# Kernel tuning notes

Measured on AMD Instinct MI355X. Metric: run time of the kernel, lower is better.

Reference implementation:

```python
import jax, jax.numpy as jnp
import numpy as np
from jax import lax

B, N, D, L, EDGE_H, NGNN = 8, 128, 256, 64, 64, 3


def setup_inputs() -> dict:
    key = jax.random.key(0)
    ks = iter(jax.random.split(key, 64))
    def nrm(shape, s=0.02):
        return jax.random.normal(next(ks), shape, jnp.float32) * s
    inp = {}
    inp["node_feats"] = jax.random.uniform(next(ks), (B, N, 11), jnp.float32)
    inp["edge_feats"] = jax.random.normal(next(ks), (B, N, N, 3), jnp.float32)
    inp["adj_mask"] = jax.random.randint(next(ks), (B, N, N), 0, 2).astype(bool)
    inp["layer_costs"] = jax.random.uniform(next(ks), (B, L), jnp.float32)
    inp["global_dynamic"] = jax.random.uniform(next(ks), (B, 2), jnp.float32)
    inp["p_node_w"] = nrm((11, D)); inp["p_node_b"] = jnp.zeros((D,), jnp.float32)
    inp["g_w1"] = nrm((NGNN, D + 3, EDGE_H)); inp["g_b1"] = jnp.zeros((NGNN, EDGE_H), jnp.float32)
    inp["g_w2"] = nrm((NGNN, EDGE_H, D)); inp["g_b2"] = jnp.zeros((NGNN, D), jnp.float32)
    inp["u_w1"] = nrm((NGNN, 3 * D, D)); inp["u_b1"] = jnp.zeros((NGNN, D), jnp.float32)
    inp["u_w2"] = nrm((NGNN, D, D)); inp["u_b2"] = jnp.zeros((NGNN, D), jnp.float32)
    inp["ln_g"] = jnp.ones((NGNN, D), jnp.float32); inp["ln_b"] = jnp.zeros((NGNN, D), jnp.float32)
    inp["conv_w"] = nrm((32, 1, 4)); inp["conv_b"] = jnp.zeros((32,), jnp.float32)
    inp["lp_w"] = nrm((32 * 31, D)); inp["lp_b"] = jnp.zeros((D,), jnp.float32)
    inp["q_w"] = nrm((2 * D + 2, D)); inp["q_b"] = jnp.zeros((D,), jnp.float32)
    inp["k_w"] = nrm((D, D)); inp["k_b"] = jnp.zeros((D,), jnp.float32)
    inp["s_w1"] = nrm((D + 2, D)); inp["s_b1"] = jnp.zeros((D,), jnp.float32)
    inp["s_w2"] = nrm((D, 1)); inp["s_b2"] = jnp.zeros((1,), jnp.float32)
    inp["v_w1"] = nrm((2 * D + 2, D)); inp["v_b1"] = jnp.zeros((D,), jnp.float32)
    inp["v_w2"] = nrm((D, 1)); inp["v_b2"] = jnp.zeros((1,), jnp.float32)
    return inp


def _ecgc(h, edge_feats, adj_bool, gw1, gb1, gw2, gb2, uw1, ub1, uw2, ub2, lng, lnb):
    Bh, Nn, Dd = h.shape
    # h_j: features of sender node j broadcast over receiver axis -> (B, N, N, D)
    h_j = jnp.broadcast_to(h[:, None, :, :], (Bh, Nn, Nn, Dd))
    gate_in = jnp.concatenate([h_j, edge_feats], axis=-1)            # (B,N,N,D+3)
    gates = jax.nn.sigmoid(jax.nn.relu(gate_in @ gw1 + gb1) @ gw2 + gb2)
    msg = gates * h_j                                                # (B,N,N,D)
    m = adj_bool.astype(h.dtype)[..., None]
    cnt = jnp.maximum(m.sum(axis=2), 1.0)                            # (B,N,1)
    agg_mean = (msg * m).sum(axis=2) / cnt                           # (B,N,D)
    agg_max = jnp.where(adj_bool[..., None], msg, -jnp.inf).max(axis=2)
    agg_max = jnp.where(jnp.isinf(agg_max), 0.0, agg_max)
    ui = jnp.concatenate([h, agg_mean, agg_max], axis=-1)            # (B,N,3D)
    x = h + (jax.nn.relu(ui @ uw1 + ub1) @ uw2 + ub2)
    mu = x.mean(-1, keepdims=True)
    var = ((x - mu) ** 2).mean(-1, keepdims=True)
    return (x - mu) * lax.rsqrt(var + 1e-5) * lng + lnb


def reference(node_feats, edge_feats, adj_mask, layer_costs, global_dynamic,
              p_node_w, p_node_b, g_w1, g_b1, g_w2, g_b2, u_w1, u_b1, u_w2, u_b2,
              ln_g, ln_b, conv_w, conv_b, lp_w, lp_b, q_w, q_b, k_w, k_b,
              s_w1, s_b1, s_w2, s_b2, v_w1, v_b1, v_w2, v_b2):
    # layer cost encoder: Conv1d(1,32,k=4,s=2) + ReLU, flatten, Linear
    le = lax.conv_general_dilated(layer_costs[:, None, :], conv_w, (2,), 'VALID',
                                  dimension_numbers=('NCH', 'OIH', 'NCH'))
    le = jax.nn.relu(le + conv_b[None, :, None])                     # (B,32,31)
    layer_embed = le.reshape(le.shape[0], -1) @ lp_w + lp_b          # (B,D)
    h = node_feats @ p_node_w + p_node_b                             # (B,N,D)
    for i in range(g_w1.shape[0]):
        h = _ecgc(h, edge_feats, adj_mask, g_w1[i], g_b1[i], g_w2[i], g_b2[i],
                  u_w1[i], u_b1[i], u_w2[i], u_b2[i], ln_g[i], ln_b[i])
    w = (node_feats[:, :, 0] * node_feats[:, :, 7])[..., None]       # (B,N,1)
    graph_embed = (w * h).sum(axis=1) / jnp.maximum(w.sum(axis=1), 1e-8)
    qi = jnp.concatenate([graph_embed, layer_embed, global_dynamic], axis=-1)
    query = qi @ q_w + q_b                                           # (B,D)
    keys = h @ k_w + k_b                                             # (B,N,D)
    device_scores = jnp.einsum('bnd,bd->bn', keys, query) / jnp.sqrt(jnp.float32(query.shape[-1]))
    si = jnp.concatenate([graph_embed, global_dynamic], axis=-1)
    stop_logit = jax.nn.relu(si @ s_w1 + s_b1) @ s_w2 + s_b2         # (B,1)
    all_logits = jnp.concatenate([device_scores, stop_logit], axis=1)
    value = jax.nn.relu(qi @ v_w1 + v_b1) @ v_w2 + v_b2              # (B,1)
    return all_logits, value, h
```

## Files before the change

### kernel.cpp

```cpp
#include <hip/hip_runtime.h>
#include <hip/hip_bf16.h>
#include <math.h>

#define BB 8
#define NN_ 128
#define DD 256
#define LL 64
#define EH 64
#define NG 3

typedef __attribute__((ext_vector_type(8))) short bs8;
typedef __attribute__((ext_vector_type(4))) float f4;

__device__ __forceinline__ short f2bf(float f) {
    __hip_bfloat16 h = __float2bfloat16(f);
    return *reinterpret_cast<short*>(&h);
}

__device__ __forceinline__ bs8 cvt8(const float* __restrict__ p) {
    bs8 r;
    #pragma unroll
    for (int i = 0; i < 8; ++i) r[i] = f2bf(p[i]);
    return r;
}

__device__ __forceinline__ float blockReduceSum(float v, float* sRed) {
    int tid = threadIdx.x;
    __syncthreads();
    sRed[tid] = v;
    __syncthreads();
    for (int s = 128; s > 0; s >>= 1) {
        if (tid < s) sRed[tid] += sRed[tid + s];
        __syncthreads();
    }
    return sRed[0];
}

__global__ __launch_bounds__(256) void k_prep(
    const float* __restrict__ uw1, const float* __restrict__ uw2,
    const float* __restrict__ gw2, const float* __restrict__ gw1,
    const float* __restrict__ kw, const unsigned char* __restrict__ adj,
    const float* __restrict__ lc, const float* __restrict__ cw,
    const float* __restrict__ cb, const float* __restrict__ lpw,
    unsigned short* __restrict__ w1t, unsigned short* __restrict__ w2t,
    unsigned short* __restrict__ g2t, unsigned short* __restrict__ g1t,
    unsigned short* __restrict__ kwt, int* __restrict__ mode,
    float* __restrict__ lpart)
{
    const int blk = blockIdx.x, tid = threadIdx.x;
    if (blk == 232) {
        __shared__ int sOff, sBig;
        if (tid == 0) { sOff = 0; sBig = 0; }
        __syncthreads();
        int off = 0, big = 0;
        #pragma unroll
        for (int k = 0; k < 4; ++k) {
            unsigned char v = adj[tid * 4 + k];
            if (v > 1) big = 1;
            if (k != 0 && v != 0) off = 1;
        }
        if (off) atomicOr(&sOff, 1);
        if (big) atomicOr(&sBig, 1);
        __syncthreads();
        if (tid == 0) mode[0] = sBig ? 2 : (sOff ? 0 : 1);
        return;
    }
    if (blk > 232) {
        const int lb = blk - 233;
        const int b = lb >> 5, kseg = (lb >> 2) & 7, c4 = lb & 3;
        const int d = tid & 63, ss = tid >> 6;
        __shared__ float sC[LL];
        __shared__ float sV[124];
        __shared__ float sP[4][64];
        if (tid < LL) sC[tid] = lc[b * LL + tid];
        __syncthreads();
        if (tid < 124) {
            int idx = kseg * 124 + tid;
            int c = idx / 31, t = idx - c * 31;
            float a = cb[c];
            #pragma unroll
            for (int k = 0; k < 4; ++k) a += sC[2 * t + k] * cw[c * 4 + k];
            sV[tid] = fmaxf(a, 0.f);
        }
        __syncthreads();
        float acc = 0.f;
        for (int k = ss; k < 124; k += 4)
            acc += sV[k] * lpw[(size_t)(kseg * 124 + k) * DD + c4 * 64 + d];
        sP[ss][d] = acc;
        __syncthreads();
        if (ss == 0)
            lpart[(b * 32 + kseg * 4 + c4) * 64 + d] = sP[0][d] + sP[1][d] + sP[2][d] + sP[3][d];
        return;
    }
    const float* src; unsigned short* dst; int K, kt, dt, srcw = 256;
    if (blk < 144)      { int l = blk / 48, t = blk % 48; kt = t >> 2; dt = t & 3;
                          src = uw1 + (size_t)l * 196608; dst = w1t + (size_t)l * 196608; K = 768; }
    else if (blk < 192) { int x = blk - 144, l = x / 16, t = x % 16; kt = t >> 2; dt = t & 3;
                          src = uw2 + (size_t)l * 65536; dst = w2t + (size_t)l * 65536; K = 256; }
    else if (blk < 204) { int x = blk - 192, l = x >> 2; kt = 0; dt = x & 3;
                          src = gw2 + (size_t)l * 16384; dst = g2t + (size_t)l * 16384; K = 64; }
    else if (blk < 216) { int x = blk - 204, l = x >> 2; kt = x & 3; dt = 0; srcw = 64;
                          src = gw1 + (size_t)l * 16576; dst = g1t + (size_t)l * 16384; K = 256; }
    else                { int x = blk - 216; kt = x >> 2; dt = x & 3;
                          src = kw; dst = kwt; K = 256; }
    __shared__ float sT[64][65];
    #pragma unroll
    for (int q = 0; q < 16; ++q) {
        int idx = q * 256 + tid, kk = idx >> 6, dd = idx & 63;
        sT[kk][dd] = src[(size_t)(kt * 64 + kk) * srcw + dt * 64 + dd];
    }
    __syncthreads();
    const int d = tid >> 2, kc = (tid & 3) * 16;
    unsigned short* drow = dst + (size_t)(dt * 64 + d) * K + kt * 64 + kc;
    #pragma unroll
    for (int i = 0; i < 16; ++i) drow[i] = (unsigned short)f2bf(sT[kc + i][d]);
}

__global__ __launch_bounds__(256) void k_npp(
    const float* __restrict__ nf, const float* __restrict__ pnw,
    const float* __restrict__ pnb,
    const unsigned short* __restrict__ g1t, const float* __restrict__ gb1,
    float* __restrict__ h, float* __restrict__ preg)
{
    const int tid = threadIdx.x, blk = blockIdx.x;
    const int row0 = blk * 16;
    const int lane = tid & 63, w = tid >> 6;
    const int lcol = lane & 15, lrow = lane >> 4;
    __shared__ float sF[16][12];
    __shared__ float sH[16][260];
    if (tid < 176) sF[tid / 11][tid % 11] = nf[(size_t)(row0 + tid / 11) * 11 + tid % 11];
    __syncthreads();
    float acc[16];
    {
        float bb = pnb[tid];
        #pragma unroll
        for (int rr = 0; rr < 16; ++rr) acc[rr] = bb;
    }
    #pragma unroll
    for (int f = 0; f < 11; ++f) {
        float wf = pnw[f * DD + tid];
        #pragma unroll
        for (int rr = 0; rr < 16; ++rr) acc[rr] += sF[rr][f] * wf;
    }
    #pragma unroll
    for (int rr = 0; rr < 16; ++rr) {
        sH[rr][tid] = acc[rr];
        h[(size_t)(row0 + rr) * DD + tid] = acc[rr];
    }
    __syncthreads();
    const unsigned short* bR = g1t + (size_t)(w * 16 + lcol) * 256;
    f4 a2 = {0.f, 0.f, 0.f, 0.f};
    #pragma unroll
    for (int ks = 0; ks < 8; ++ks) {
        int k0 = ks * 32 + lrow * 8;
        bs8 av = cvt8(&sH[lcol][k0]);
        bs8 bv = *(const bs8*)(bR + k0);
        a2 = __builtin_amdgcn_mfma_f32_16x16x32_bf16(av, bv, a2, 0, 0, 0);
    }
    const float gb = gb1[w * 16 + lcol];
    #pragma unroll
    for (int r = 0; r < 4; ++r)
        preg[(size_t)(row0 + lrow * 4 + r) * EH + w * 16 + lcol] = a2[r] + gb;
}

__global__ __launch_bounds__(256) void k_edge(
    const float* __restrict__ h, const float* __restrict__ preg,
    const float* __restrict__ edge, const void* __restrict__ adj,
    const int* __restrict__ mode,
    const float* __restrict__ gw1,
    const unsigned short* __restrict__ g2t,
    const float* __restrict__ gb2,
    float* __restrict__ agg_mean, float* __restrict__ agg_max)
{
    const int tid = threadIdx.x;
    const int bi = blockIdx.x;
    const int b = bi >> 7;
    const int lane = tid & 63, w = tid >> 6;
    const int lrow = lane >> 4, lcol = lane & 15;
    const int md = mode[0];

    __shared__ __align__(16) unsigned int sHid[4096];
    __shared__ float sWe[192];
    __shared__ float sE[384];
    __shared__ unsigned long long sMask[2];

    if (tid < 192) sWe[tid] = gw1[16384 + tid];
    const float* eB = edge + (size_t)bi * 384;
    for (int idx = tid; idx < 384; idx += 256) sE[idx] = eB[idx];
    if (tid < 128) {
        int mv;
        if (md == 1)      mv = ((const int*)adj)[(size_t)bi * NN_ + tid] != 0;
        else if (md == 2) mv = ((const float*)adj)[(size_t)bi * NN_ + tid] != 0.f;
        else              mv = ((const unsigned char*)adj)[(size_t)bi * NN_ + tid] != 0;
        unsigned long long bal = __ballot(mv);
        if ((tid & 63) == 0) sMask[tid >> 6] = bal;
    }
    __syncthreads();

    const float* pB = preg + (size_t)b * NN_ * EH;
    #pragma unroll
    for (int q = 0; q < 16; ++q) {
        int idx = q * 256 + tid;
        int j = idx >> 5, p = idx & 31;
        float2 pv = *(const float2*)(pB + j * EH + 2 * p);
        float e0 = sE[j * 3], e1 = sE[j * 3 + 1], e2 = sE[j * 3 + 2];
        int t0 = 2 * p, t1 = t0 + 1;
        float v0 = fmaxf(pv.x + e0 * sWe[t0] + e1 * sWe[64 + t0] + e2 * sWe[128 + t0], 0.f);
        float v1 = fmaxf(pv.y + e0 * sWe[t1] + e1 * sWe[64 + t1] + e2 * sWe[128 + t1], 0.f);
        unsigned int pk = (unsigned int)(unsigned short)f2bf(v0) |
                          ((unsigned int)(unsigned short)f2bf(v1) << 16);
        sHid[j * 32 + (p ^ ((j & 7) << 2))] = pk;
    }
    __syncthreads();

    const unsigned long long m0 = sMask[0], m1 = sMask[1];
    const float cntf = (float)(__popcll(m0) + __popcll(m1));

    bs8 bfr[4][2];
    float bg[4];
    #pragma unroll
    for (int nt = 0; nt < 4; ++nt) {
        int d = w * 64 + nt * 16 + lcol;
        bg[nt] = gb2[d];
        #pragma unroll
        for (int ks = 0; ks < 2; ++ks) {
            int k0 = ks * 32 + lrow * 8;
            bfr[nt][ks] = *(const bs8*)(g2t + (size_t)d * 64 + k0);
        }
    }

    const float* hB = h + (size_t)b * NN_ * DD;
    float vs[4] = {0.f, 0.f, 0.f, 0.f};
    float vm[4] = {-INFINITY, -INFINITY, -INFINITY, -INFINITY};

    #pragma unroll
    for (int pp = 0; pp < 2; ++pp) {
        f4 acc[4][4] = {};
        #pragma unroll
        for (int ks = 0; ks < 2; ++ks) {
            bs8 afr[4];
            #pragma unroll
            for (int m = 0; m < 4; ++m) {
                int j = pp * 64 + m * 16 + lcol;
                int k0 = ks * 32 + lrow * 8;
                afr[m] = *(const bs8*)(sHid + (j * 32 + ((k0 >> 1) ^ ((j & 7) << 2))));
            }
            #pragma unroll
            for (int m = 0; m < 4; ++m)
                #pragma unroll
                for (int nt = 0; nt < 4; ++nt)
                    acc[m][nt] = __builtin_amdgcn_mfma_f32_16x16x32_bf16(
                        afr[m], bfr[nt][ks], acc[m][nt], 0, 0, 0);
        }
        const unsigned long long mw = pp ? m1 : m0;
        #pragma unroll
        for (int m = 0; m < 4; ++m) {
            #pragma unroll
            for (int nt = 0; nt < 4; ++nt) {
                int dnt = w * 64 + nt * 16 + lcol;
                #pragma unroll
                for (int r = 0; r < 4; ++r) {
                    int bit = m * 16 + lrow * 4 + r;
                    float x = acc[m][nt][r] + bg[nt];
                    float g = __builtin_amdgcn_rcpf(1.0f + __expf(-x));
                    float msg = g * hB[(pp * 64 + bit) * DD + dnt];
                    int on = (int)((mw >> bit) & 1ULL);
                    vs[nt] += on ? msg : 0.f;
                    vm[nt] = fmaxf(vm[nt], on ? msg : -INFINITY);
                }
            }
        }
    }

    #pragma unroll
    for (int nt = 0; nt < 4; ++nt) {
        float s = vs[nt];
        s += __shfl_xor(s, 16); s += __shfl_xor(s, 32);
        vs[nt] = s;
        float m = vm[nt];
        m = fmaxf(m, __shfl_xor(m, 16)); m = fmaxf(m, __shfl_xor(m, 32));
        vm[nt] = m;
    }
    const int g = lrow;
    float ssel = (g == 0) ? vs[0] : (g == 1) ? vs[1] : (g == 2) ? vs[2] : vs[3];
    float msel = (g == 0) ? vm[0] : (g == 1) ? vm[1] : (g == 2) ? vm[2] : vm[3];
    const int d = w * 64 + lane;
    agg_mean[(size_t)bi * DD + d] = ssel / fmaxf(cntf, 1.f);
    agg_max[(size_t)bi * DD + d] = (cntf > 0.f) ? msel : 0.f;
}

__global__ __launch_bounds__(256) void k_updp(
    const float* __restrict__ h, const float* __restrict__ amean,
    const float* __restrict__ amax,
    const unsigned short* __restrict__ w1t,
    const float* __restrict__ ub1,
    const unsigned short* __restrict__ w2t,
    const float* __restrict__ ub2,
    const float* __restrict__ lng, const float* __restrict__ lnb,
    float* __restrict__ hout, float* __restrict__ out2,
    const unsigned short* __restrict__ g1tn, const float* __restrict__ gb1n,
    float* __restrict__ preg)
{
    const int tid = threadIdx.x;
    const int row0 = blockIdx.x * 4;
    const int lane = tid & 63, w = tid >> 6;
    const int lcol = lane & 15, lrow = lane >> 4;

    __shared__ __align__(16) unsigned int sX32[16 * 384];
    __shared__ __align__(16) unsigned short sH16[16 * 256];
    __shared__ float sRes[4][256];
    __shared__ float sOut[4][260];

    {
        const int j = w;
        const float* hR = h + (size_t)(row0 + j) * DD;
        const float* mR = amean + (size_t)(row0 + j) * DD;
        const float* xR = amax + (size_t)(row0 + j) * DD;
        #pragma unroll
        for (int q = 0; q < 6; ++q) {
            int p = lane + q * 64;
            int k = 2 * p;
            float2 v;
            if (k < 256)      { v = *(const float2*)(hR + k); sRes[j][k] = v.x; sRes[j][k + 1] = v.y; }
            else if (k < 512)   v = *(const float2*)(mR + (k - 256));
            else                v = *(const float2*)(xR + (k - 512));
            unsigned int pk = (unsigned int)(unsigned short)f2bf(v.x) |
                              ((unsigned int)(unsigned short)f2bf(v.y) << 16);
            sX32[j * 384 + (p ^ (j << 2))] = pk;
        }
    }
    __syncthreads();

    const char* sXb = (const char*)sX32;
    const unsigned short* w1r = w1t + (size_t)(w * 64 + lcol) * 768;
    f4 a0 = {0.f, 0.f, 0.f, 0.f}, a1 = a0, a2 = a0, a3 = a0;
    #pragma unroll 4
    for (int ks = 0; ks < 24; ++ks) {
        int k0 = ks * 32 + lrow * 8;
        bs8 av = *(const bs8*)(sXb + lcol * 1536 + ((((k0 >> 3) ^ (lcol & 7))) << 4));
        bs8 b0 = *(const bs8*)(w1r + k0);
        bs8 b1 = *(const bs8*)(w1r + 16 * 768 + k0);
        bs8 b2 = *(const bs8*)(w1r + 32 * 768 + k0);
        bs8 b3 = *(const bs8*)(w1r + 48 * 768 + k0);
        a0 = __builtin_amdgcn_mfma_f32_16x16x32_bf16(av, b0, a0, 0, 0, 0);
        a1 = __builtin_amdgcn_mfma_f32_16x16x32_bf16(av, b1, a1, 0, 0, 0);
        a2 = __builtin_amdgcn_mfma_f32_16x16x32_bf16(av, b2, a2, 0, 0, 0);
        a3 = __builtin_amdgcn_mfma_f32_16x16x32_bf16(av, b3, a3, 0, 0, 0);
    }
    if (lrow == 0) {
        #pragma unroll
        for (int nt = 0; nt < 4; ++nt) {
            int d = w * 64 + nt * 16 + lcol;
            float bb = ub1[d];
            f4 A = (nt == 0) ? a0 : (nt == 1) ? a1 : (nt == 2) ? a2 : a3;
            #pragma unroll
            for (int r = 0; r < 4; ++r) {
                float hv = fmaxf(A[r] + bb, 0.f);
                sH16[r * 256 + (d ^ (r << 3))] = (unsigned short)f2bf(hv);
            }
        }
    }
    __syncthreads();

    const unsigned short* w2r = w2t + (size_t)(w * 64 + lcol) * 256;
    f4 c0 = {0.f, 0.f, 0.f, 0.f}, c1 = c0, c2 = c0, c3 = c0;
    #pragma unroll
    for (int ks = 0; ks < 8; ++ks) {
        int k0 = ks * 32 + lrow * 8;
        bs8 av = *(const bs8*)((const char*)sH16 + lcol * 512 + ((((k0 >> 3) ^ (lcol & 7))) << 4));
        bs8 b0 = *(const bs8*)(w2r + k0);
        bs8 b1 = *(const bs8*)(w2r + 16 * 256 + k0);
        bs8 b2 = *(const bs8*)(w2r + 32 * 256 + k0);
        bs8 b3 = *(const bs8*)(w2r + 48 * 256 + k0);
        c0 = __builtin_amdgcn_mfma_f32_16x16x32_bf16(av, b0, c0, 0, 0, 0);
        c1 = __builtin_amdgcn_mfma_f32_16x16x32_bf16(av, b1, c1, 0, 0, 0);
        c2 = __builtin_amdgcn_mfma_f32_16x16x32_bf16(av, b2, c2, 0, 0, 0);
        c3 = __builtin_amdgcn_mfma_f32_16x16x32_bf16(av, b3, c3, 0, 0, 0);
    }
    if (lrow == 0) {
        #pragma unroll
        for (int nt = 0; nt < 4; ++nt) {
            int d = w * 64 + nt * 16 + lcol;
            float bb = ub2[d];
            f4 C = (nt == 0) ? c0 : (nt == 1) ? c1 : (nt == 2) ? c2 : c3;
            #pragma unroll
            for (int r = 0; r < 4; ++r)
                sOut[r][d] = C[r] + bb + sRes[r][d];
        }
    }
    __syncthreads();

    float xv[4], s = 0.f;
    #pragma unroll
    for (int q = 0; q < 4; ++q) { xv[q] = sOut[w][lane + 64 * q]; s += xv[q]; }
    #pragma unroll
    for (int off = 1; off < 64; off <<= 1) s += __shfl_xor(s, off);
    const float mu = s * (1.f / DD);
    float s2 = 0.f;
    #pragma unroll
    for (int q = 0; q < 4; ++q) { float d = xv[q] - mu; s2 += d * d; }
    #pragma unroll
    for (int off = 1; off < 64; off <<= 1) s2 += __shfl_xor(s2, off);
    const float inv = rsqrtf(s2 * (1.f / DD) + 1e-5f);
    #pragma unroll
    for (int q = 0; q < 4; ++q) {
        int c = lane + 64 * q;
        float res = (xv[q] - mu) * inv * lng[c] + lnb[c];
        hout[(size_t)(row0 + w) * DD + c] = res;
        if (out2) out2[(size_t)(row0 + w) * DD + c] = res;
        sOut[w][c] = res;
    }
    if (g1tn) {
        __syncthreads();
        const unsigned short* bR = g1tn + (size_t)(w * 16 + lcol) * 256;
        f4 p = {0.f, 0.f, 0.f, 0.f};
        #pragma unroll
        for (int ks = 0; ks < 8; ++ks) {
            int k0 = ks * 32 + lrow * 8;
            bs8 av = cvt8(&sOut[lcol & 3][k0]);
            bs8 bv = *(const bs8*)(bR + k0);
            p = __builtin_amdgcn_mfma_f32_16x16x32_bf16(av, bv, p, 0, 0, 0);
        }
        if (lrow == 0) {
            const float gb = gb1n[w * 16 + lcol];
            #pragma unroll
            for (int r = 0; r < 4; ++r)
                preg[(size_t)(row0 + r) * EH + w * 16 + lcol] = p[r] + gb;
        }
    }
}

__global__ __launch_bounds__(256) void k_gembed(
    const float* __restrict__ nf, const float* __restrict__ h, float* __restrict__ ge)
{
    const int b = blockIdx.x, tid = threadIdx.x;
    __shared__ float sW[NN_];
    __shared__ float sRed[256];
    if (tid < NN_) {
        const float* p = nf + ((size_t)b * NN_ + tid) * 11;
        sW[tid] = p[0] * p[7];
    }
    __syncthreads();
    float part = (tid < NN_) ? sW[tid] : 0.f;
    float wsum = blockReduceSum(part, sRed);
    const float* hb = h + (size_t)b * NN_ * DD + tid;
    float a0 = 0.f, a1 = 0.f, a2 = 0.f, a3 = 0.f;
    for (int n = 0; n < 32; ++n) {
        a0 += sW[n]      * hb[(size_t)n * DD];
        a1 += sW[n + 32] * hb[(size_t)(n + 32) * DD];
        a2 += sW[n + 64] * hb[(size_t)(n + 64) * DD];
        a3 += sW[n + 96] * hb[(size_t)(n + 96) * DD];
    }
    ge[b * DD + tid] = (a0 + a1 + a2 + a3) / fmaxf(wsum, 1e-8f);
}

__global__ __launch_bounds__(256) void k_hmm(
    const float* __restrict__ ge, const float* __restrict__ gd,
    const float* __restrict__ qw, const float* __restrict__ sw1,
    const float* __restrict__ vw1,
    const float* __restrict__ lpb, const float* __restrict__ lpart,
    float* __restrict__ part)
{
    const int blk = blockIdx.x;
    const int m = blk >> 5, kseg = (blk >> 2) & 7, c4 = blk & 3;
    const int tid = threadIdx.x;
    const int d = tid & 63, ks = tid >> 6;
    const int K = (m == 1) ? 258 : 514;
    const int kc = (m == 1) ? 33 : 65;
    const int k0 = kseg * kc;
    const int klen = min(k0 + kc, K) - k0;
    __shared__ float sX[8 * 66];
    __shared__ float sP[4][8][64];
    for (int idx = tid; idx < 8 * kc; idx += 256) {
        int bb = idx / kc, kk = idx % kc, k = k0 + kk;
        float v = 0.f;
        if (k < K) {
            if (m == 1) v = (k < 256) ? ge[bb * DD + k] : gd[bb * 2 + (k - 256)];
            else if (k < 256) v = ge[bb * DD + k];
            else if (k < 512) {
                int e = k - 256;
                v = lpb[e];
                #pragma unroll
                for (int s = 0; s < 8; ++s)
                    v += lpart[(bb * 32 + s * 4 + (e >> 6)) * 64 + (e & 63)];
            } else v = gd[bb * 2 + (k - 512)];
        }
        sX[bb * 66 + kk] = v;
    }
    __syncthreads();
    const float* W = (m == 0) ? qw : (m == 1) ? sw1 : vw1;
    const int dg = c4 * 64 + d;
    float acc[8] = {0.f, 0.f, 0.f, 0.f, 0.f, 0.f, 0.f, 0.f};
    for (int kk = ks; kk < klen; kk += 4) {
        float wv = W[(size_t)(k0 + kk) * DD + dg];
        #pragma unroll
        for (int bb = 0; bb < 8; ++bb) acc[bb] += sX[bb * 66 + kk] * wv;
    }
    #pragma unroll
    for (int bb = 0; bb < 8; ++bb) sP[ks][bb][d] = acc[bb];
    __syncthreads();
    for (int idx = tid; idx < 8 * 64; idx += 256) {
        int bb = idx >> 6, dd = idx & 63;
        float sum = sP[0][bb][dd] + sP[1][bb][dd] + sP[2][bb][dd] + sP[3][bb][dd];
        part[((m * 8 + kseg) * 8 + bb) * DD + c4 * 64 + dd] = sum;
    }
}

__global__ __launch_bounds__(256) void k_scr(
    const float* __restrict__ h, const unsigned short* __restrict__ kwt,
    const float* __restrict__ kb, const float* __restrict__ hpart,
    const float* __restrict__ qb,
    const float* __restrict__ sb1, const float* __restrict__ vb1,
    const float* __restrict__ sw2, const float* __restrict__ sb2,
    const float* __restrict__ vw2, const float* __restrict__ vb2,
    float* __restrict__ out)
{
    const int tid = threadIdx.x, blk = blockIdx.x;
    const int row0 = blk * 16, b = blk >> 3, chunk = blk & 7;
    const int lane = tid & 63, w = tid >> 6;
    const int lcol = lane & 15, lrow = lane >> 4;
    __shared__ float sQ[256];
    __shared__ float sPart[4][16];
    __shared__ float sRed[256];
    {
        float qv = qb[tid];
        #pragma unroll
        for (int kseg = 0; kseg < 8; ++kseg)
            qv += hpart[(size_t)(kseg * 8 + b) * DD + tid];
        sQ[tid] = qv;
    }
    __syncthreads();
    const float* aR = h + (size_t)(row0 + lcol) * DD;
    f4 acc[4] = {};
    #pragma unroll
    for (int ks = 0; ks < 8; ++ks) {
        int k0 = ks * 32 + lrow * 8;
        bs8 av = cvt8(aR + k0);
        #pragma unroll
        for (int nt = 0; nt < 4; ++nt) {
            bs8 bv = *(const bs8*)(kwt + (size_t)(w * 64 + nt * 16 + lcol) * 256 + k0);
            acc[nt] = __builtin_amdgcn_mfma_f32_16x16x32_bf16(av, bv, acc[nt], 0, 0, 0);
        }
    }
    float part[4] = {0.f, 0.f, 0.f, 0.f};
    #pragma unroll
    for (int nt = 0; nt < 4; ++nt) {
        int col = w * 64 + nt * 16 + lcol;
        float q = sQ[col], kv = kb[col];
        #pragma unroll
        for (int r = 0; r < 4; ++r) part[r] += (acc[nt][r] + kv) * q;
    }
    #pragma unroll
    for (int r = 0; r < 4; ++r) {
        float s = part[r];
        s += __shfl_xor(s, 1); s += __shfl_xor(s, 2);
        s += __shfl_xor(s, 4); s += __shfl_xor(s, 8);
        part[r] = s;
    }
    if (lcol == 0) {
        #pragma unroll
        for (int r = 0; r < 4; ++r) sPart[w][lrow * 4 + r] = part[r];
    }
    __syncthreads();
    if (tid < 16) {
        float s = sPart[0][tid] + sPart[1][tid] + sPart[2][tid] + sPart[3][tid];
        out[b * 129 + (row0 & (NN_ - 1)) + tid] = s * 0.0625f;
    }
    if (chunk == 0) {
        float s = sb1[tid], v = vb1[tid];
        #pragma unroll
        for (int kseg = 0; kseg < 8; ++kseg) {
            s += hpart[(size_t)((8 + kseg) * 8 + b) * DD + tid];
            v += hpart[(size_t)((16 + kseg) * 8 + b) * DD + tid];
        }
        s = fmaxf(s, 0.f); v = fmaxf(v, 0.f);
        float stop = blockReduceSum(s * sw2[tid], sRed);
        float val  = blockReduceSum(v * vw2[tid], sRed);
        if (tid == 0) {
            out[b * 129 + 128] = stop + sb2[0];
            out[1032 + b] = val + vb2[0];
        }
    }
}

extern "C" void kernel_launch(void* const* d_in, const int* in_sizes, int n_in,
                              void* d_out, int out_size, void* d_ws, size_t ws_size,
                              hipStream_t stream) {
    (void)in_sizes; (void)n_in; (void)out_size; (void)ws_size;
    const float* nf  = (const float*)d_in[0];
    const float* ef  = (const float*)d_in[1];
    const void*  adj = d_in[2];
    const float* lc  = (const float*)d_in[3];
    const float* gd  = (const float*)d_in[4];
    const float* pnw = (const float*)d_in[5];
    const float* pnb = (const float*)d_in[6];
    const float* gw1 = (const float*)d_in[7];
    const float* gb1 = (const float*)d_in[8];
    const float* gw2 = (const float*)d_in[9];
    const float* gb2 = (const float*)d_in[10];
    const float* uw1 = (const float*)d_in[11];
    const float* ub1 = (const float*)d_in[12];
    const float* uw2 = (const float*)d_in[13];
    const float* ub2 = (const float*)d_in[14];
    const float* lng = (const float*)d_in[15];
    const float* lnb = (const float*)d_in[16];
    const float* cw  = (const float*)d_in[17];
    const float* cb  = (const float*)d_in[18];
    const float* lpw = (const float*)d_in[19];
    const float* lpb = (const float*)d_in[20];
    const float* qw  = (const float*)d_in[21];
    const float* qb  = (const float*)d_in[22];
    const float* kw  = (const float*)d_in[23];
    const float* kb  = (const float*)d_in[24];
    const float* sw1 = (const float*)d_in[25];
    const float* sb1 = (const float*)d_in[26];
    const float* sw2 = (const float*)d_in[27];
    const float* sb2 = (const float*)d_in[28];
    const float* vw1 = (const float*)d_in[29];
    const float* vb1 = (const float*)d_in[30];
    const float* vw2 = (const float*)d_in[31];
    const float* vb2 = (const float*)d_in[32];

    float* ws = (float*)d_ws;
    float* h     = ws;
    float* preg  = ws + 262144;
    float* amean = ws + 327680;
    float* amax  = ws + 589824;
    float* ge    = ws + 851968;
    float* lpart = ws + 856064;
    float* hpart = ws + 872448;
    int*   mode  = (int*)(ws + 921600);
    unsigned short* uw1t = (unsigned short*)(ws + 921604);
    unsigned short* uw2t = (unsigned short*)(ws + 1216516);
    unsigned short* g2t  = (unsigned short*)(ws + 1314820);
    unsigned short* g1t  = (unsigned short*)(ws + 1339396);
    unsigned short* kwt  = (unsigned short*)(ws + 1363972);
    float* out   = (float*)d_out;

    k_prep<<<489, 256, 0, stream>>>(uw1, uw2, gw2, gw1, kw,
                                    (const unsigned char*)adj,
                                    lc, cw, cb, lpw,
                                    uw1t, uw2t, g2t, g1t, kwt, mode, lpart);
    k_npp<<<BB * NN_ / 16, 256, 0, stream>>>(nf, pnw, pnb, g1t, gb1, h, preg);
    for (int i = 0; i < NG; ++i) {
        const float* gw1i = gw1 + (size_t)i * 259 * EH;
        float* out2sel = (i == NG - 1) ? (out + 1040) : (float*)nullptr;
        const unsigned short* g1tn = (i < NG - 1) ? (g1t + (size_t)(i + 1) * 16384)
                                                  : (const unsigned short*)nullptr;
        const float* gb1n = (i < NG - 1) ? (gb1 + (i + 1) * EH) : (const float*)nullptr;
        k_edge<<<BB * NN_, 256, 0, stream>>>(h, preg, ef, adj, mode, gw1i,
                                             g2t + (size_t)i * 16384,
                                             gb2 + i * DD, amean, amax);
        k_updp<<<BB * NN_ / 4, 256, 0, stream>>>(h, amean, amax,
                                                 uw1t + (size_t)i * 196608, ub1 + i * DD,
                                                 uw2t + (size_t)i * 65536, ub2 + i * DD,
                                                 lng + i * DD, lnb + i * DD, h, out2sel,
                                                 g1tn, gb1n, preg);
    }
    k_gembed<<<BB, 256, 0, stream>>>(nf, h, ge);
    k_hmm<<<96, 256, 0, stream>>>(ge, gd, qw, sw1, vw1, lpb, lpart, hpart);
    k_scr<<<BB * NN_ / 16, 256, 0, stream>>>(h, kwt, kb, hpart, qb, sb1, vb1,
                                             sw2, sb2, vw2, vb2, out);
}
```

Before: 183.9 us.

## Fuse GNN layers and heads into one persistent kernel with grid barriers

```diff
diff --git a/kernel.cpp b/kernel.cpp
--- a/kernel.cpp
+++ b/kernel.cpp
@@ -8,6 +8,7 @@
 #define LL 64
 #define EH 64
 #define NG 3
+#define NBLK 256
 
 typedef __attribute__((ext_vector_type(8))) short bs8;
 typedef __attribute__((ext_vector_type(4))) float f4;
@@ -36,20 +37,40 @@
     return sRed[0];
 }
 
+__device__ __forceinline__ void gbar(int* cnt, int* gen) {
+    __syncthreads();
+    if (threadIdx.x == 0) {
+        __threadfence();
+        int g = __hip_atomic_load(gen, __ATOMIC_RELAXED, __HIP_MEMORY_SCOPE_AGENT);
+        int v = __hip_atomic_fetch_add(cnt, 1, __ATOMIC_ACQ_REL, __HIP_MEMORY_SCOPE_AGENT);
+        if (v == NBLK - 1) {
+            __hip_atomic_store(cnt, 0, __ATOMIC_RELAXED, __HIP_MEMORY_SCOPE_AGENT);
+            __hip_atomic_fetch_add(gen, 1, __ATOMIC_RELEASE, __HIP_MEMORY_SCOPE_AGENT);
+        } else {
+            while (__hip_atomic_load(gen, __ATOMIC_ACQUIRE, __HIP_MEMORY_SCOPE_AGENT) == g)
+                __builtin_amdgcn_s_sleep(2);
+        }
+        __threadfence();
+    }
+    __syncthreads();
+}
+
 __global__ __launch_bounds__(256) void k_prep(
     const float* __restrict__ uw1, const float* __restrict__ uw2,
     const float* __restrict__ gw2, const float* __restrict__ gw1,
     const float* __restrict__ kw, const unsigned char* __restrict__ adj,
     const float* __restrict__ lc, const float* __restrict__ cw,
     const float* __restrict__ cb, const float* __restrict__ lpw,
+    const float* __restrict__ nf,
     unsigned short* __restrict__ w1t, unsigned short* __restrict__ w2t,
     unsigned short* __restrict__ g2t, unsigned short* __restrict__ g1t,
     unsigned short* __restrict__ kwt, int* __restrict__ mode,
-    float* __restrict__ lpart)
+    float* __restrict__ lpart, float* __restrict__ wsum, int* __restrict__ cnt)
 {
     const int blk = blockIdx.x, tid = threadIdx.x;
     if (blk == 232) {
         __shared__ int sOff, sBig;
+        __shared__ float sRedD[256];
         if (tid == 0) { sOff = 0; sBig = 0; }
         __syncthreads();
         int off = 0, big = 0;
@@ -62,7 +83,16 @@
         if (off) atomicOr(&sOff, 1);
         if (big) atomicOr(&sBig, 1);
         __syncthreads();
-        if (tid == 0) mode[0] = sBig ? 2 : (sOff ? 0 : 1);
+        if (tid == 0) { mode[0] = sBig ? 2 : (sOff ? 0 : 1); *cnt = 0; }
+        for (int bb = 0; bb < 8; ++bb) {
+            float v = 0.f;
+            if (tid < 128) {
+                const float* p = nf + (size_t)(bb * 128 + tid) * 11;
+                v = p[0] * p[7];
+            }
+            float s = blockReduceSum(v, sRedD);
+            if (tid == 0) wsum[bb] = s;
+        }
         return;
     }
     if (blk > 232) {
@@ -116,303 +146,49 @@
     for (int i = 0; i < 16; ++i) drow[i] = (unsigned short)f2bf(sT[kc + i][d]);
 }
 
-__global__ __launch_bounds__(256) void k_npp(
-    const float* __restrict__ nf, const float* __restrict__ pnw,
-    const float* __restrict__ pnb,
-    const unsigned short* __restrict__ g1t, const float* __restrict__ gb1,
-    float* __restrict__ h, float* __restrict__ preg)
+__global__ __launch_bounds__(256, 1) void k_mega(
+    const float* __restrict__ nf, const float* __restrict__ ef,
+    const void* __restrict__ adj, const float* __restrict__ gd,
+    const float* __restrict__ pnw, const float* __restrict__ pnb,
+    const float* __restrict__ gw1, const float* __restrict__ gb1,
+    const float* __restrict__ gb2,
+    const float* __restrict__ ub1, const float* __restrict__ ub2,
+    const float* __restrict__ lng, const float* __restrict__ lnb,
+    const float* __restrict__ qw, const float* __restrict__ sw1,
+    const float* __restrict__ vw1,
+    const float* __restrict__ qb, const float* __restrict__ sb1,
+    const float* __restrict__ vb1,
+    const float* __restrict__ sw2, const float* __restrict__ sb2,
+    const float* __restrict__ vw2, const float* __restrict__ vb2,
+    const float* __restrict__ kb, const float* __restrict__ lpb,
+    float* __restrict__ h, float* __restrict__ preg,
+    const float* __restrict__ lpart, float* __restrict__ hpart,
+    float* __restrict__ gpart, const float* __restrict__ wsum,
+    const int* __restrict__ mode, int* __restrict__ cnt, int* __restrict__ gen,
+    const unsigned short* __restrict__ uw1t, const unsigned short* __restrict__ uw2t,
+    const unsigned short* __restrict__ g2t, const unsigned short* __restrict__ g1t,
+    const unsigned short* __restrict__ kwt, float* __restrict__ out)
 {
-    const int tid = threadIdx.x, blk = blockIdx.x;
-    const int row0 = blk * 16;
+    const int bid = blockIdx.x, tid = threadIdx.x;
     const int lane = tid & 63, w = tid >> 6;
     const int lcol = lane & 15, lrow = lane >> 4;
-    __shared__ float sF[16][12];
-    __shared__ float sH[16][260];
-    if (tid < 176) sF[tid / 11][tid % 11] = nf[(size_t)(row0 + tid / 11) * 11 + tid % 11];
-    __syncthreads();
-    float acc[16];
-    {
-        float bb = pnb[tid];
-        #pragma unroll
-        for (int rr = 0; rr < 16; ++rr) acc[rr] = bb;
-    }
-    #pragma unroll
-    for (int f = 0; f < 11; ++f) {
-        float wf = pnw[f * DD + tid];
-        #pragma unroll
-        for (int rr = 0; rr < 16; ++rr) acc[rr] += sF[rr][f] * wf;
-    }
-    #pragma unroll
-    for (int rr = 0; rr < 16; ++rr) {
-        sH[rr][tid] = acc[rr];
-        h[(size_t)(row0 + rr) * DD + tid] = acc[rr];
-    }
-    __syncthreads();
-    const unsigned short* bR = g1t + (size_t)(w * 16 + lcol) * 256;
-    f4 a2 = {0.f, 0.f, 0.f, 0.f};
-    #pragma unroll
-    for (int ks = 0; ks < 8; ++ks) {
-        int k0 = ks * 32 + lrow * 8;
-        bs8 av = cvt8(&sH[lcol][k0]);
-        bs8 bv = *(const bs8*)(bR + k0);
-        a2 = __builtin_amdgcn_mfma_f32_16x16x32_bf16(av, bv, a2, 0, 0, 0);
-    }
-    const float gb = gb1[w * 16 + lcol];
-    #pragma unroll
-    for (int r = 0; r < 4; ++r)
-        preg[(size_t)(row0 + lrow * 4 + r) * EH + w * 16 + lcol] = a2[r] + gb;
-}
-
-__global__ __launch_bounds__(256) void k_edge(
-    const float* __restrict__ h, const float* __restrict__ preg,
-    const float* __restrict__ edge, const void* __restrict__ adj,
-    const int* __restrict__ mode,
-    const float* __restrict__ gw1,
-    const unsigned short* __restrict__ g2t,
-    const float* __restrict__ gb2,
-    float* __restrict__ agg_mean, float* __restrict__ agg_max)
-{
-    const int tid = threadIdx.x;
-    const int bi = blockIdx.x;
-    const int b = bi >> 7;
-    const int lane = tid & 63, w = tid >> 6;
-    const int lrow = lane >> 4, lcol = lane & 15;
+    const int row0 = bid * 4;
+    const int b = row0 >> 7;
     const int md = mode[0];
 
-    __shared__ __align__(16) unsigned int sHid[4096];
-    __shared__ float sWe[192];
-    __shared__ float sE[384];
-    __shared__ unsigned long long sMask[2];
-
-    if (tid < 192) sWe[tid] = gw1[16384 + tid];
-    const float* eB = edge + (size_t)bi * 384;
-    for (int idx = tid; idx < 384; idx += 256) sE[idx] = eB[idx];
-    if (tid < 128) {
-        int mv;
-        if (md == 1)      mv = ((const int*)adj)[(size_t)bi * NN_ + tid] != 0;
-        else if (md == 2) mv = ((const float*)adj)[(size_t)bi * NN_ + tid] != 0.f;
-        else              mv = ((const unsigned char*)adj)[(size_t)bi * NN_ + tid] != 0;
-        unsigned long long bal = __ballot(mv);
-        if ((tid & 63) == 0) sMask[tid >> 6] = bal;
-    }
-    __syncthreads();
-
-    const float* pB = preg + (size_t)b * NN_ * EH;
-    #pragma unroll
-    for (int q = 0; q < 16; ++q) {
-        int idx = q * 256 + tid;
-        int j = idx >> 5, p = idx & 31;
-        float2 pv = *(const float2*)(pB + j * EH + 2 * p);
-        float e0 = sE[j * 3], e1 = sE[j * 3 + 1], e2 = sE[j * 3 + 2];
-        int t0 = 2 * p, t1 = t0 + 1;
-        float v0 = fmaxf(pv.x + e0 * sWe[t0] + e1 * sWe[64 + t0] + e2 * sWe[128 + t0], 0.f);
-        float v1 = fmaxf(pv.y + e0 * sWe[t1] + e1 * sWe[64 + t1] + e2 * sWe[128 + t1], 0.f);
-        unsigned int pk = (unsigned int)(unsigned short)f2bf(v0) |
-                          ((unsigned int)(unsigned short)f2bf(v1) << 16);
-        sHid[j * 32 + (p ^ ((j & 7) << 2))] = pk;
-    }
-    __syncthreads();
-
-    const unsigned long long m0 = sMask[0], m1 = sMask[1];
-    const float cntf = (float)(__popcll(m0) + __popcll(m1));
-
-    bs8 bfr[4][2];
-    float bg[4];
-    #pragma unroll
-    for (int nt = 0; nt < 4; ++nt) {
-        int d = w * 64 + nt * 16 + lcol;
-        bg[nt] = gb2[d];
-        #pragma unroll
-        for (int ks = 0; ks < 2; ++ks) {
-            int k0 = ks * 32 + lrow * 8;
-            bfr[nt][ks] = *(const bs8*)(g2t + (size_t)d * 64 + k0);
-        }
-    }
-
-    const float* hB = h + (size_t)b * NN_ * DD;
-    float vs[4] = {0.f, 0.f, 0.f, 0.f};
-    float vm[4] = {-INFINITY, -INFINITY, -INFINITY, -INFINITY};
-
-    #pragma unroll
-    for (int pp = 0; pp < 2; ++pp) {
-        f4 acc[4][4] = {};
-        #pragma unroll
-        for (int ks = 0; ks < 2; ++ks) {
-            bs8 afr[4];
-            #pragma unroll
-            for (int m = 0; m < 4; ++m) {
-                int j = pp * 64 + m * 16 + lcol;
-                int k0 = ks * 32 + lrow * 8;
-                afr[m] = *(const bs8*)(sHid + (j * 32 + ((k0 >> 1) ^ ((j & 7) << 2))));
-            }
-            #pragma unroll
-            for (int m = 0; m < 4; ++m)
-                #pragma unroll
-                for (int nt = 0; nt < 4; ++nt)
-                    acc[m][nt] = __builtin_amdgcn_mfma_f32_16x16x32_bf16(
-                        afr[m], bfr[nt][ks], acc[m][nt], 0, 0, 0);
-        }
-        const unsigned long long mw = pp ? m1 : m0;
-        #pragma unroll
-        for (int m = 0; m < 4; ++m) {
-            #pragma unroll
-            for (int nt = 0; nt < 4; ++nt) {
-                int dnt = w * 64 + nt * 16 + lcol;
-                #pragma unroll
-                for (int r = 0; r < 4; ++r) {
-                    int bit = m * 16 + lrow * 4 + r;
-                    float x = acc[m][nt][r] + bg[nt];
-                    float g = __builtin_amdgcn_rcpf(1.0f + __expf(-x));
-                    float msg = g * hB[(pp * 64 + bit) * DD + dnt];
-                    int on = (int)((mw >> bit) & 1ULL);
-                    vs[nt] += on ? msg : 0.f;
-                    vm[nt] = fmaxf(vm[nt], on ? msg : -INFINITY);
-                }
-            }
-        }
-    }
-
-    #pragma unroll
-    for (int nt = 0; nt < 4; ++nt) {
-        float s = vs[nt];
-        s += __shfl_xor(s, 16); s += __shfl_xor(s, 32);
-        vs[nt] = s;
-        float m = vm[nt];
-        m = fmaxf(m, __shfl_xor(m, 16)); m = fmaxf(m, __shfl_xor(m, 32));
-        vm[nt] = m;
-    }
-    const int g = lrow;
-    float ssel = (g == 0) ? vs[0] : (g == 1) ? vs[1] : (g == 2) ? vs[2] : vs[3];
-    float msel = (g == 0) ? vm[0] : (g == 1) ? vm[1] : (g == 2) ? vm[2] : vm[3];
-    const int d = w * 64 + lane;
-    agg_mean[(size_t)bi * DD + d] = ssel / fmaxf(cntf, 1.f);
-    agg_max[(size_t)bi * DD + d] = (cntf > 0.f) ? msel : 0.f;
-}
-
-__global__ __launch_bounds__(256) void k_updp(
-    const float* __restrict__ h, const float* __restrict__ amean,
-    const float* __restrict__ amax,
-    const unsigned short* __restrict__ w1t,
-    const float* __restrict__ ub1,
-    const unsigned short* __restrict__ w2t,
-    const float* __restrict__ ub2,
-    const float* __restrict__ lng, const float* __restrict__ lnb,
-    float* __restrict__ hout, float* __restrict__ out2,
-    const unsigned short* __restrict__ g1tn, const float* __restrict__ gb1n,
-    float* __restrict__ preg)
-{
-    const int tid = threadIdx.x;
-    const int row0 = blockIdx.x * 4;
-    const int lane = tid & 63, w = tid >> 6;
-    const int lcol = lane & 15, lrow = lane >> 4;
-
-    __shared__ __align__(16) unsigned int sX32[16 * 384];
-    __shared__ __align__(16) unsigned short sH16[16 * 256];
+    __shared__ __align__(16) char regA[32768];
+    __shared__ float aggM[4][256];
+    __shared__ float aggX[4][256];
     __shared__ float sRes[4][256];
     __shared__ float sOut[4][260];
-
-    {
-        const int j = w;
-        const float* hR = h + (size_t)(row0 + j) * DD;
-        const float* mR = amean + (size_t)(row0 + j) * DD;
-        const float* xR = amax + (size_t)(row0 + j) * DD;
-        #pragma unroll
-        for (int q = 0; q < 6; ++q) {
-            int p = lane + q * 64;
-            int k = 2 * p;
-            float2 v;
-            if (k < 256)      { v = *(const float2*)(hR + k); sRes[j][k] = v.x; sRes[j][k + 1] = v.y; }
-            else if (k < 512)   v = *(const float2*)(mR + (k - 256));
-            else                v = *(const float2*)(xR + (k - 512));
-            unsigned int pk = (unsigned int)(unsigned short)f2bf(v.x) |
-                              ((unsigned int)(unsigned short)f2bf(v.y) << 16);
-            sX32[j * 384 + (p ^ (j << 2))] = pk;
-        }
-    }
-    __syncthreads();
-
-    const char* sXb = (const char*)sX32;
-    const unsigned short* w1r = w1t + (size_t)(w * 64 + lcol) * 768;
-    f4 a0 = {0.f, 0.f, 0.f, 0.f}, a1 = a0, a2 = a0, a3 = a0;
-    #pragma unroll 4
-    for (int ks = 0; ks < 24; ++ks) {
-        int k0 = ks * 32 + lrow * 8;
-        bs8 av = *(const bs8*)(sXb + lcol * 1536 + ((((k0 >> 3) ^ (lcol & 7))) << 4));
-        bs8 b0 = *(const bs8*)(w1r + k0);
-        bs8 b1 = *(const bs8*)(w1r + 16 * 768 + k0);
-        bs8 b2 = *(const bs8*)(w1r + 32 * 768 + k0);
-        bs8 b3 = *(const bs8*)(w1r + 48 * 768 + k0);
-        a0 = __builtin_amdgcn_mfma_f32_16x16x32_bf16(av, b0, a0, 0, 0, 0);
-        a1 = __builtin_amdgcn_mfma_f32_16x16x32_bf16(av, b1, a1, 0, 0, 0);
-        a2 = __builtin_amdgcn_mfma_f32_16x16x32_bf16(av, b2, a2, 0, 0, 0);
-        a3 = __builtin_amdgcn_mfma_f32_16x16x32_bf16(av, b3, a3, 0, 0, 0);
-    }
-    if (lrow == 0) {
-        #pragma unroll
-        for (int nt = 0; nt < 4; ++nt) {
-            int d = w * 64 + nt * 16 + lcol;
-            float bb = ub1[d];
-            f4 A = (nt == 0) ? a0 : (nt == 1) ? a1 : (nt == 2) ? a2 : a3;
-            #pragma unroll
-            for (int r = 0; r < 4; ++r) {
-                float hv = fmaxf(A[r] + bb, 0.f);
-                sH16[r * 256 + (d ^ (r << 3))] = (unsigned short)f2bf(hv);
-            }
-        }
-    }
-    __syncthreads();
-
-    const unsigned short* w2r = w2t + (size_t)(w * 64 + lcol) * 256;
-    f4 c0 = {0.f, 0.f, 0.f, 0.f}, c1 = c0, c2 = c0, c3 = c0;
-    #pragma unroll
-    for (int ks = 0; ks < 8; ++ks) {
-        int k0 = ks * 32 + lrow * 8;
-        bs8 av = *(const bs8*)((const char*)sH16 + lcol * 512 + ((((k0 >> 3) ^ (lcol & 7))) << 4));
-        bs8 b0 = *(const bs8*)(w2r + k0);
-        bs8 b1 = *(const bs8*)(w2r + 16 * 256 + k0);
-        bs8 b2 = *(const bs8*)(w2r + 32 * 256 + k0);
-        bs8 b3 = *(const bs8*)(w2r + 48 * 256 + k0);
-        c0 = __builtin_amdgcn_mfma_f32_16x16x32_bf16(av, b0, c0, 0, 0, 0);
-        c1 = __builtin_amdgcn_mfma_f32_16x16x32_bf16(av, b1, c1, 0, 0, 0);
-        c2 = __builtin_amdgcn_mfma_f32_16x16x32_bf16(av, b2, c2, 0, 0, 0);
-        c3 = __builtin_amdgcn_mfma_f32_16x16x32_bf16(av, b3, c3, 0, 0, 0);
-    }
-    if (lrow == 0) {
-        #pragma unroll
-        for (int nt = 0; nt < 4; ++nt) {
-            int d = w * 64 + nt * 16 + lcol;
-            float bb = ub2[d];
-            f4 C = (nt == 0) ? c0 : (nt == 1) ? c1 : (nt == 2) ? c2 : c3;
-            #pragma unroll
-            for (int r = 0; r < 4; ++r)
-                sOut[r][d] = C[r] + bb + sRes[r][d];
-        }
-    }
-    __syncthreads();
-
-    float xv[4], s = 0.f;
-    #pragma unroll
-    for (int q = 0; q < 4; ++q) { xv[q] = sOut[w][lane + 64 * q]; s += xv[q]; }
-    #pragma unroll
-    for (int off = 1; off < 64; off <<= 1) s += __shfl_xor(s, off);
-    const float mu = s * (1.f / DD);
-    float s2 = 0.f;
-    #pragma unroll
-    for (int q = 0; q < 4; ++q) { float d = xv[q] - mu; s2 += d * d; }
-    #pragma unroll
-    for (int off = 1; off < 64; off <<= 1) s2 += __shfl_xor(s2, off);
-    const float inv = rsqrtf(s2 * (1.f / DD) + 1e-5f);
-    #pragma unroll
-    for (int q = 0; q < 4; ++q) {
-        int c = lane + 64 * q;
-        float res = (xv[q] - mu) * inv * lng[c] + lnb[c];
-        hout[(size_t)(row0 + w) * DD + c] = res;
-        if (out2) out2[(size_t)(row0 + w) * DD + c] = res;
-        sOut[w][c] = res;
-    }
-    if (g1tn) {
-        __syncthreads();
-        const unsigned short* bR = g1tn + (size_t)(w * 16 + lcol) * 256;
+    __shared__ float sWe[192];
+    __shared__ float sE[4][384];
+    __shared__ unsigned long long sMask[4][2];
+    __shared__ float sWr[4];
+    __shared__ float sF[4][11];
+
+    auto pregateF = [&](const unsigned short* g1, const float* gb) {
+        const unsigned short* bR = g1 + (size_t)(w * 16 + lcol) * 256;
         f4 p = {0.f, 0.f, 0.f, 0.f};
         #pragma unroll
         for (int ks = 0; ks < 8; ++ks) {
@@ -422,163 +198,384 @@
             p = __builtin_amdgcn_mfma_f32_16x16x32_bf16(av, bv, p, 0, 0, 0);
         }
         if (lrow == 0) {
-            const float gb = gb1n[w * 16 + lcol];
+            const float gb_ = gb[w * 16 + lcol];
             #pragma unroll
             for (int r = 0; r < 4; ++r)
-                preg[(size_t)(row0 + r) * EH + w * 16 + lcol] = p[r] + gb;
-        }
-    }
-}
-
-__global__ __launch_bounds__(256) void k_gembed(
-    const float* __restrict__ nf, const float* __restrict__ h, float* __restrict__ ge)
-{
-    const int b = blockIdx.x, tid = threadIdx.x;
-    __shared__ float sW[NN_];
-    __shared__ float sRed[256];
-    if (tid < NN_) {
-        const float* p = nf + ((size_t)b * NN_ + tid) * 11;
-        sW[tid] = p[0] * p[7];
+                preg[(size_t)(row0 + r) * EH + w * 16 + lcol] = p[r] + gb_;
+        }
+    };
+
+    if (tid < 44) sF[tid / 11][tid % 11] = nf[(size_t)(row0 + tid / 11) * 11 + tid % 11];
+    if (tid < 4) {
+        const float* p = nf + (size_t)(row0 + tid) * 11;
+        sWr[tid] = p[0] * p[7];
     }
     __syncthreads();
-    float part = (tid < NN_) ? sW[tid] : 0.f;
-    float wsum = blockReduceSum(part, sRed);
-    const float* hb = h + (size_t)b * NN_ * DD + tid;
-    float a0 = 0.f, a1 = 0.f, a2 = 0.f, a3 = 0.f;
-    for (int n = 0; n < 32; ++n) {
-        a0 += sW[n]      * hb[(size_t)n * DD];
-        a1 += sW[n + 32] * hb[(size_t)(n + 32) * DD];
-        a2 += sW[n + 64] * hb[(size_t)(n + 64) * DD];
-        a3 += sW[n + 96] * hb[(size_t)(n + 96) * DD];
-    }
-    ge[b * DD + tid] = (a0 + a1 + a2 + a3) / fmaxf(wsum, 1e-8f);
-}
-
-__global__ __launch_bounds__(256) void k_hmm(
-    const float* __restrict__ ge, const float* __restrict__ gd,
-    const float* __restrict__ qw, const float* __restrict__ sw1,
-    const float* __restrict__ vw1,
-    const float* __restrict__ lpb, const float* __restrict__ lpart,
-    float* __restrict__ part)
-{
-    const int blk = blockIdx.x;
-    const int m = blk >> 5, kseg = (blk >> 2) & 7, c4 = blk & 3;
-    const int tid = threadIdx.x;
-    const int d = tid & 63, ks = tid >> 6;
-    const int K = (m == 1) ? 258 : 514;
-    const int kc = (m == 1) ? 33 : 65;
-    const int k0 = kseg * kc;
-    const int klen = min(k0 + kc, K) - k0;
-    __shared__ float sX[8 * 66];
-    __shared__ float sP[4][8][64];
-    for (int idx = tid; idx < 8 * kc; idx += 256) {
-        int bb = idx / kc, kk = idx % kc, k = k0 + kk;
-        float v = 0.f;
-        if (k < K) {
-            if (m == 1) v = (k < 256) ? ge[bb * DD + k] : gd[bb * 2 + (k - 256)];
-            else if (k < 256) v = ge[bb * DD + k];
-            else if (k < 512) {
-                int e = k - 256;
-                v = lpb[e];
+    {
+        float a0 = pnb[tid], a1 = a0, a2 = a0, a3 = a0;
+        #pragma unroll
+        for (int f = 0; f < 11; ++f) {
+            float wf = pnw[f * DD + tid];
+            a0 += sF[0][f] * wf; a1 += sF[1][f] * wf;
+            a2 += sF[2][f] * wf; a3 += sF[3][f] * wf;
+        }
+        h[(size_t)(row0 + 0) * DD + tid] = a0; sRes[0][tid] = a0; sOut[0][tid] = a0;
+        h[(size_t)(row0 + 1) * DD + tid] = a1; sRes[1][tid] = a1; sOut[1][tid] = a1;
+        h[(size_t)(row0 + 2) * DD + tid] = a2; sRes[2][tid] = a2; sOut[2][tid] = a2;
+        h[(size_t)(row0 + 3) * DD + tid] = a3; sRes[3][tid] = a3; sOut[3][tid] = a3;
+    }
+    __syncthreads();
+    pregateF(g1t, gb1);
+    gbar(cnt, gen);
+
+    unsigned int* const buf0 = (unsigned int*)regA;
+    unsigned int* const buf1 = (unsigned int*)(regA + 16384);
+    const float* const pB = preg + (size_t)b * NN_ * EH;
+    const float* const hB = h + (size_t)b * NN_ * DD;
+
+    auto hidStage = [&](unsigned int* dst, int n) {
+        #pragma unroll
+        for (int q = 0; q < 16; ++q) {
+            int idx = q * 256 + tid;
+            int j = idx >> 5, p = idx & 31;
+            float2 pv = *(const float2*)(pB + j * EH + 2 * p);
+            float e0 = sE[n][j * 3], e1 = sE[n][j * 3 + 1], e2 = sE[n][j * 3 + 2];
+            int t0 = 2 * p, t1 = t0 + 1;
+            float v0 = fmaxf(pv.x + e0 * sWe[t0] + e1 * sWe[64 + t0] + e2 * sWe[128 + t0], 0.f);
+            float v1 = fmaxf(pv.y + e0 * sWe[t1] + e1 * sWe[64 + t1] + e2 * sWe[128 + t1], 0.f);
+            unsigned int pk = (unsigned int)(unsigned short)f2bf(v0) |
+                              ((unsigned int)(unsigned short)f2bf(v1) << 16);
+            dst[j * 32 + (p ^ ((j & 7) << 2))] = pk;
+        }
+    };
+
+    for (int L = 0; L < NG; ++L) {
+        if (tid < 192) sWe[tid] = gw1[(size_t)L * 16576 + 16384 + tid];
+        for (int idx = tid; idx < 4 * 384; idx += 256) {
+            int n = idx / 384, e = idx - n * 384;
+            sE[n][e] = ef[(size_t)(row0 + n) * 384 + e];
+        }
+        #pragma unroll
+        for (int n = 0; n < 4; ++n) {
+            if (tid < 128) {
+                size_t ai = (size_t)(row0 + n) * NN_ + tid;
+                int mv;
+                if (md == 1)      mv = ((const int*)adj)[ai] != 0;
+                else if (md == 2) mv = ((const float*)adj)[ai] != 0.f;
+                else              mv = ((const unsigned char*)adj)[ai] != 0;
+                unsigned long long bal = __ballot(mv);
+                if ((tid & 63) == 0) sMask[n][tid >> 6] = bal;
+            }
+        }
+        bs8 bfr[4][2];
+        float bg[4];
+        const unsigned short* g2L = g2t + (size_t)L * 16384;
+        #pragma unroll
+        for (int nt = 0; nt < 4; ++nt) {
+            int d = w * 64 + nt * 16 + lcol;
+            bg[nt] = gb2[L * DD + d];
+            #pragma unroll
+            for (int ks = 0; ks < 2; ++ks)
+                bfr[nt][ks] = *(const bs8*)(g2L + (size_t)d * 64 + ks * 32 + lrow * 8);
+        }
+        __syncthreads();
+        hidStage(buf0, 0);
+        __syncthreads();
+        int cur = 0;
+        #pragma unroll
+        for (int n = 0; n < 4; ++n) {
+            if (n < 3) hidStage(cur ? buf0 : buf1, n + 1);
+            {
+                const unsigned int* sHid = cur ? buf1 : buf0;
+                const unsigned long long m0 = sMask[n][0], m1 = sMask[n][1];
+                const float cntf = (float)(__popcll(m0) + __popcll(m1));
+                float vs[4] = {0.f, 0.f, 0.f, 0.f};
+                float vm[4] = {-INFINITY, -INFINITY, -INFINITY, -INFINITY};
                 #pragma unroll
-                for (int s = 0; s < 8; ++s)
-                    v += lpart[(bb * 32 + s * 4 + (e >> 6)) * 64 + (e & 63)];
-            } else v = gd[bb * 2 + (k - 512)];
-        }
-        sX[bb * 66 + kk] = v;
-    }
-    __syncthreads();
-    const float* W = (m == 0) ? qw : (m == 1) ? sw1 : vw1;
-    const int dg = c4 * 64 + d;
-    float acc[8] = {0.f, 0.f, 0.f, 0.f, 0.f, 0.f, 0.f, 0.f};
-    for (int kk = ks; kk < klen; kk += 4) {
-        float wv = W[(size_t)(k0 + kk) * DD + dg];
-        #pragma unroll
-        for (int bb = 0; bb < 8; ++bb) acc[bb] += sX[bb * 66 + kk] * wv;
-    }
-    #pragma unroll
-    for (int bb = 0; bb < 8; ++bb) sP[ks][bb][d] = acc[bb];
-    __syncthreads();
-    for (int idx = tid; idx < 8 * 64; idx += 256) {
-        int bb = idx >> 6, dd = idx & 63;
-        float sum = sP[0][bb][dd] + sP[1][bb][dd] + sP[2][bb][dd] + sP[3][bb][dd];
-        part[((m * 8 + kseg) * 8 + bb) * DD + c4 * 64 + dd] = sum;
-    }
-}
-
-__global__ __launch_bounds__(256) void k_scr(
-    const float* __restrict__ h, const unsigned short* __restrict__ kwt,
-    const float* __restrict__ kb, const float* __restrict__ hpart,
-    const float* __restrict__ qb,
-    const float* __restrict__ sb1, const float* __restrict__ vb1,
-    const float* __restrict__ sw2, const float* __restrict__ sb2,
-    const float* __restrict__ vw2, const float* __restrict__ vb2,
-    float* __restrict__ out)
-{
-    const int tid = threadIdx.x, blk = blockIdx.x;
-    const int row0 = blk * 16, b = blk >> 3, chunk = blk & 7;
-    const int lane = tid & 63, w = tid >> 6;
-    const int lcol = lane & 15, lrow = lane >> 4;
-    __shared__ float sQ[256];
-    __shared__ float sPart[4][16];
-    __shared__ float sRed[256];
-    {
-        float qv = qb[tid];
-        #pragma unroll
-        for (int kseg = 0; kseg < 8; ++kseg)
-            qv += hpart[(size_t)(kseg * 8 + b) * DD + tid];
-        sQ[tid] = qv;
-    }
-    __syncthreads();
-    const float* aR = h + (size_t)(row0 + lcol) * DD;
-    f4 acc[4] = {};
-    #pragma unroll
-    for (int ks = 0; ks < 8; ++ks) {
-        int k0 = ks * 32 + lrow * 8;
-        bs8 av = cvt8(aR + k0);
+                for (int pp = 0; pp < 2; ++pp) {
+                    f4 acc[4][4] = {};
+                    #pragma unroll
+                    for (int ks = 0; ks < 2; ++ks) {
+                        bs8 afr[4];
+                        #pragma unroll
+                        for (int m = 0; m < 4; ++m) {
+                            int j = pp * 64 + m * 16 + lcol;
+                            int k0 = ks * 32 + lrow * 8;
+                            afr[m] = *(const bs8*)(sHid + (j * 32 + ((k0 >> 1) ^ ((j & 7) << 2))));
+                        }
+                        #pragma unroll
+                        for (int m = 0; m < 4; ++m)
+                            #pragma unroll
+                            for (int nt = 0; nt < 4; ++nt)
+                                acc[m][nt] = __builtin_amdgcn_mfma_f32_16x16x32_bf16(
+                                    afr[m], bfr[nt][ks], acc[m][nt], 0, 0, 0);
+                    }
+                    const unsigned long long mw = pp ? m1 : m0;
+                    #pragma unroll
+                    for (int m = 0; m < 4; ++m) {
+                        #pragma unroll
+                        for (int nt = 0; nt < 4; ++nt) {
+                            int dnt = w * 64 + nt * 16 + lcol;
+                            #pragma unroll
+                            for (int r = 0; r < 4; ++r) {
+                                int bit = m * 16 + lrow * 4 + r;
+                                float x = acc[m][nt][r] + bg[nt];
+                                float g = __builtin_amdgcn_rcpf(1.0f + __expf(-x));
+                                float msg = g * hB[(pp * 64 + bit) * DD + dnt];
+                                int on = (int)((mw >> bit) & 1ULL);
+                                vs[nt] += on ? msg : 0.f;
+                                vm[nt] = fmaxf(vm[nt], on ? msg : -INFINITY);
+                            }
+                        }
+                    }
+                }
+                #pragma unroll
+                for (int nt = 0; nt < 4; ++nt) {
+                    float s = vs[nt];
+                    s += __shfl_xor(s, 16); s += __shfl_xor(s, 32);
+                    vs[nt] = s;
+                    float m = vm[nt];
+                    m = fmaxf(m, __shfl_xor(m, 16)); m = fmaxf(m, __shfl_xor(m, 32));
+                    vm[nt] = m;
+                }
+                const int g = lrow;
+                float ssel = (g == 0) ? vs[0] : (g == 1) ? vs[1] : (g == 2) ? vs[2] : vs[3];
+                float msel = (g == 0) ? vm[0] : (g == 1) ? vm[1] : (g == 2) ? vm[2] : vm[3];
+                const int d = w * 64 + lane;
+                aggM[n][d] = ssel / fmaxf(cntf, 1.f);
+                aggX[n][d] = (cntf > 0.f) ? msel : 0.f;
+            }
+            cur ^= 1;
+            __syncthreads();
+        }
+
+        unsigned int* sX32 = (unsigned int*)regA;
+        unsigned short* sH16 = (unsigned short*)(regA + 24576);
+        {
+            const int j = w;
+            #pragma unroll
+            for (int q = 0; q < 6; ++q) {
+                int p = lane + q * 64;
+                int k = 2 * p;
+                float v0, v1;
+                if (k < 256)      { v0 = sRes[j][k]; v1 = sRes[j][k + 1]; }
+                else if (k < 512) { v0 = aggM[j][k - 256]; v1 = aggM[j][k - 255]; }
+                else              { v0 = aggX[j][k - 512]; v1 = aggX[j][k - 511]; }
+                unsigned int pk = (unsigned int)(unsigned short)f2bf(v0) |
+                                  ((unsigned int)(unsigned short)f2bf(v1) << 16);
+                sX32[j * 384 + (p ^ (j << 2))] = pk;
+            }
+        }
+        __syncthreads();
+        const char* sXb = (const char*)sX32;
+        const unsigned short* w1r = uw1t + (size_t)L * 196608 + (size_t)(w * 64 + lcol) * 768;
+        f4 a0 = {0.f, 0.f, 0.f, 0.f}, a1 = a0, a2 = a0, a3 = a0;
+        #pragma unroll 4
+        for (int ks = 0; ks < 24; ++ks) {
+            int k0 = ks * 32 + lrow * 8;
+            bs8 av = *(const bs8*)(sXb + lcol * 1536 + ((((k0 >> 3) ^ (lcol & 7))) << 4));
+            bs8 b0 = *(const bs8*)(w1r + k0);
+            bs8 b1 = *(const bs8*)(w1r + 16 * 768 + k0);
+            bs8 b2 = *(const bs8*)(w1r + 32 * 768 + k0);
+            bs8 b3 = *(const bs8*)(w1r + 48 * 768 + k0);
+            a0 = __builtin_amdgcn_mfma_f32_16x16x32_bf16(av, b0, a0, 0, 0, 0);
+            a1 = __builtin_amdgcn_mfma_f32_16x16x32_bf16(av, b1, a1, 0, 0, 0);
+            a2 = __builtin_amdgcn_mfma_f32_16x16x32_bf16(av, b2, a2, 0, 0, 0);
+            a3 = __builtin_amdgcn_mfma_f32_16x16x32_bf16(av, b3, a3, 0, 0, 0);
+        }
+        if (lrow == 0) {
+            #pragma unroll
+            for (int nt = 0; nt < 4; ++nt) {
+                int d = w * 64 + nt * 16 + lcol;
+                float bb = ub1[L * DD + d];
+                f4 A = (nt == 0) ? a0 : (nt == 1) ? a1 : (nt == 2) ? a2 : a3;
+                #pragma unroll
+                for (int r = 0; r < 4; ++r) {
+                    float hv = fmaxf(A[r] + bb, 0.f);
+                    sH16[r * 256 + (d ^ (r << 3))] = (unsigned short)f2bf(hv);
+                }
+            }
+        }
+        __syncthreads();
+        const unsigned short* w2r = uw2t + (size_t)L * 65536 + (size_t)(w * 64 + lcol) * 256;
+        f4 c0 = {0.f, 0.f, 0.f, 0.f}, c1 = c0, c2 = c0, c3 = c0;
+        #pragma unroll
+        for (int ks = 0; ks < 8; ++ks) {
+            int k0 = ks * 32 + lrow * 8;
+            bs8 av = *(const bs8*)((const char*)sH16 + lcol * 512 + ((((k0 >> 3) ^ (lcol & 7))) << 4));
+            bs8 b0 = *(const bs8*)(w2r + k0);
+            bs8 b1 = *(const bs8*)(w2r + 16 * 256 + k0);
+            bs8 b2 = *(const bs8*)(w2r + 32 * 256 + k0);
+            bs8 b3 = *(const bs8*)(w2r + 48 * 256 + k0);
+            c0 = __builtin_amdgcn_mfma_f32_16x16x32_bf16(av, b0, c0, 0, 0, 0);
+            c1 = __builtin_amdgcn_mfma_f32_16x16x32_bf16(av, b1, c1, 0, 0, 0);
+            c2 = __builtin_amdgcn_mfma_f32_16x16x32_bf16(av, b2, c2, 0, 0, 0);
+            c3 = __builtin_amdgcn_mfma_f32_16x16x32_bf16(av, b3, c3, 0, 0, 0);
+        }
+        if (lrow == 0) {
+            #pragma unroll
+            for (int nt = 0; nt < 4; ++nt) {
+                int d = w * 64 + nt * 16 + lcol;
+                float bb = ub2[L * DD + d];
+                f4 C = (nt == 0) ? c0 : (nt == 1) ? c1 : (nt == 2) ? c2 : c3;
+                #pragma unroll
+                for (int r = 0; r < 4; ++r)
+                    sOut[r][d] = C[r] + bb + sRes[r][d];
+            }
+        }
+        __syncthreads();
+        {
+            float xv[4], s = 0.f;
+            #pragma unroll
+            for (int q = 0; q < 4; ++q) { xv[q] = sOut[w][lane + 64 * q]; s += xv[q]; }
+            #pragma unroll
+            for (int off = 1; off < 64; off <<= 1) s += __shfl_xor(s, off);
+            const float mu = s * (1.f / DD);
+            float s2 = 0.f;
+            #pragma unroll
+            for (int q = 0; q < 4; ++q) { float d = xv[q] - mu; s2 += d * d; }
+            #pragma unroll
+            for (int off = 1; off < 64; off <<= 1) s2 += __shfl_xor(s2, off);
+            const float inv = rsqrtf(s2 * (1.f / DD) + 1e-5f);
+            #pragma unroll
+            for (int q = 0; q < 4; ++q) {
+                int c = lane + 64 * q;
+                float res = (xv[q] - mu) * inv * lng[L * DD + c] + lnb[L * DD + c];
+                h[(size_t)(row0 + w) * DD + c] = res;
+                sRes[w][c] = res;
+                sOut[w][c] = res;
+                if (L == NG - 1) out[1040 + (size_t)(row0 + w) * DD + c] = res;
+            }
+        }
+        __syncthreads();
+        if (L < NG - 1) {
+            pregateF(g1t + (size_t)(L + 1) * 16384, gb1 + (L + 1) * EH);
+        } else {
+            float g = sWr[0] * sOut[0][tid] + sWr[1] * sOut[1][tid] +
+                      sWr[2] * sOut[2][tid] + sWr[3] * sOut[3][tid];
+            gpart[(size_t)bid * DD + tid] = g;
+        }
+        gbar(cnt, gen);
+    }
+
+    if (bid < 96) {
+        const int m = bid >> 5, kseg = (bid >> 2) & 7, c4 = bid & 3;
+        const int d = tid & 63, ks = tid >> 6;
+        const int K = (m == 1) ? 258 : 514;
+        const int kc = (m == 1) ? 33 : 65;
+        const int k0 = kseg * kc;
+        const int klen = min(k0 + kc, K) - k0;
+        float* sX = (float*)regA;
+        float* sP = (float*)(regA + 4096);
+        for (int idx = tid; idx < 8 * kc; idx += 256) {
+            int bb = idx / kc, kk = idx - bb * kc, k = k0 + kk;
+            float v = 0.f;
+            if (k < K) {
+                if (k < 256) {
+                    float s = 0.f;
+                    #pragma unroll 8
+                    for (int t = 0; t < 32; ++t)
+                        s += gpart[(size_t)(bb * 32 + t) * DD + k];
+                    v = s / fmaxf(wsum[bb], 1e-8f);
+                } else if (m == 1) {
+                    v = gd[bb * 2 + (k - 256)];
+                } else if (k < 512) {
+                    int e = k - 256;
+                    v = lpb[e];
+                    #pragma unroll
+                    for (int s = 0; s < 8; ++s)
+                        v += lpart[(bb * 32 + s * 4 + (e >> 6)) * 64 + (e & 63)];
+                } else {
+                    v = gd[bb * 2 + (k - 512)];
+                }
+            }
+            sX[bb * 66 + kk] = v;
+        }
+        __syncthreads();
+        const float* W = (m == 0) ? qw : (m == 1) ? sw1 : vw1;
+        const int dg = c4 * 64 + d;
+        float acc[8] = {0.f, 0.f, 0.f, 0.f, 0.f, 0.f, 0.f, 0.f};
+        for (int kk = ks; kk < klen; kk += 4) {
+            float wv = W[(size_t)(k0 + kk) * DD + dg];
+            #pragma unroll
+            for (int bb = 0; bb < 8; ++bb) acc[bb] += sX[bb * 66 + kk] * wv;
+        }
+        #pragma unroll
+        for (int bb = 0; bb < 8; ++bb) sP[(ks * 8 + bb) * 64 + d] = acc[bb];
+        __syncthreads();
+        for (int idx = tid; idx < 8 * 64; idx += 256) {
+            int bb = idx >> 6, dd = idx & 63;
+            float sum = sP[(0 * 8 + bb) * 64 + dd] + sP[(1 * 8 + bb) * 64 + dd] +
+                        sP[(2 * 8 + bb) * 64 + dd] + sP[(3 * 8 + bb) * 64 + dd];
+            hpart[((m * 8 + kseg) * 8 + bb) * DD + c4 * 64 + dd] = sum;
+        }
+    }
+    gbar(cnt, gen);
+
+    if (bid < 64) {
+        const int srow0 = bid * 16, bs = bid >> 3, chunk = bid & 7;
+        float* sQ = (float*)regA;
+        float* sPart = (float*)(regA + 1024);
+        float* sRed = (float*)(regA + 2048);
+        {
+            float qv = qb[tid];
+            #pragma unroll
+            for (int kseg = 0; kseg < 8; ++kseg)
+                qv += hpart[(size_t)(kseg * 8 + bs) * DD + tid];
+            sQ[tid] = qv;
+        }
+        __syncthreads();
+        const float* aR = h + (size_t)(srow0 + lcol) * DD;
+        f4 acc[4] = {};
+        #pragma unroll
+        for (int ks = 0; ks < 8; ++ks) {
+            int k0 = ks * 32 + lrow * 8;
+            bs8 av = cvt8(aR + k0);
+            #pragma unroll
+            for (int nt = 0; nt < 4; ++nt) {
+                bs8 bv = *(const bs8*)(kwt + (size_t)(w * 64 + nt * 16 + lcol) * 256 + k0);
+                acc[nt] = __builtin_amdgcn_mfma_f32_16x16x32_bf16(av, bv, acc[nt], 0, 0, 0);
+            }
+        }
+        float part[4] = {0.f, 0.f, 0.f, 0.f};
         #pragma unroll
         for (int nt = 0; nt < 4; ++nt) {
-            bs8 bv = *(const bs8*)(kwt + (size_t)(w * 64 + nt * 16 + lcol) * 256 + k0);
-            acc[nt] = __builtin_amdgcn_mfma_f32_16x16x32_bf16(av, bv, acc[nt], 0, 0, 0);
-        }
-    }
-    float part[4] = {0.f, 0.f, 0.f, 0.f};
-    #pragma unroll
-    for (int nt = 0; nt < 4; ++nt) {
-        int col = w * 64 + nt * 16 + lcol;
-        float q = sQ[col], kv = kb[col];
-        #pragma unroll
-        for (int r = 0; r < 4; ++r) part[r] += (acc[nt][r] + kv) * q;
-    }
-    #pragma unroll
-    for (int r = 0; r < 4; ++r) {
-        float s = part[r];
-        s += __shfl_xor(s, 1); s += __shfl_xor(s, 2);
-        s += __shfl_xor(s, 4); s += __shfl_xor(s, 8);
-        part[r] = s;
-    }
-    if (lcol == 0) {
-        #pragma unroll
-        for (int r = 0; r < 4; ++r) sPart[w][lrow * 4 + r] = part[r];
-    }
-    __syncthreads();
-    if (tid < 16) {
-        float s = sPart[0][tid] + sPart[1][tid] + sPart[2][tid] + sPart[3][tid];
-        out[b * 129 + (row0 & (NN_ - 1)) + tid] = s * 0.0625f;
-    }
-    if (chunk == 0) {
-        float s = sb1[tid], v = vb1[tid];
-        #pragma unroll
-        for (int kseg = 0; kseg < 8; ++kseg) {
-            s += hpart[(size_t)((8 + kseg) * 8 + b) * DD + tid];
-            v += hpart[(size_t)((16 + kseg) * 8 + b) * DD + tid];
-        }
-        s = fmaxf(s, 0.f); v = fmaxf(v, 0.f);
-        float stop = blockReduceSum(s * sw2[tid], sRed);
-        float val  = blockReduceSum(v * vw2[tid], sRed);
-        if (tid == 0) {
-            out[b * 129 + 128] = stop + sb2[0];
-            out[1032 + b] = val + vb2[0];
+            int col = w * 64 + nt * 16 + lcol;
+            float q = sQ[col], kv = kb[col];
+            #pragma unroll
+            for (int r = 0; r < 4; ++r) part[r] += (acc[nt][r] + kv) * q;
+        }
+        #pragma unroll
+        for (int r = 0; r < 4; ++r) {
+            float s = part[r];
+            s += __shfl_xor(s, 1); s += __shfl_xor(s, 2);
+            s += __shfl_xor(s, 4); s += __shfl_xor(s, 8);
+            part[r] = s;
+        }
+        if (lcol == 0) {
+            #pragma unroll
+            for (int r = 0; r < 4; ++r) sPart[w * 16 + lrow * 4 + r] = part[r];
+        }
+        __syncthreads();
+        if (tid < 16) {
+            float s = sPart[0 * 16 + tid] + sPart[1 * 16 + tid] +
+                      sPart[2 * 16 + tid] + sPart[3 * 16 + tid];
+            out[bs * 129 + (srow0 & (NN_ - 1)) + tid] = s * 0.0625f;
+        }
+        if (chunk == 0) {
+            float s = sb1[tid], v = vb1[tid];
+            #pragma unroll
+            for (int kseg = 0; kseg < 8; ++kseg) {
+                s += hpart[(size_t)((8 + kseg) * 8 + bs) * DD + tid];
+                v += hpart[(size_t)((16 + kseg) * 8 + bs) * DD + tid];
+            }
+            s = fmaxf(s, 0.f); v = fmaxf(v, 0.f);
+            float stop = blockReduceSum(s * sw2[tid], sRed);
+            float val  = blockReduceSum(v * vw2[tid], sRed);
+            if (tid == 0) {
+                out[bs * 129 + 128] = stop + sb2[0];
+                out[1032 + bs] = val + vb2[0];
+            }
         }
     }
 }
@@ -624,41 +621,28 @@
     float* ws = (float*)d_ws;
     float* h     = ws;
     float* preg  = ws + 262144;
-    float* amean = ws + 327680;
-    float* amax  = ws + 589824;
-    float* ge    = ws + 851968;
-    float* lpart = ws + 856064;
-    float* hpart = ws + 872448;
-    int*   mode  = (int*)(ws + 921600);
-    unsigned short* uw1t = (unsigned short*)(ws + 921604);
-    unsigned short* uw2t = (unsigned short*)(ws + 1216516);
-    unsigned short* g2t  = (unsigned short*)(ws + 1314820);
-    unsigned short* g1t  = (unsigned short*)(ws + 1339396);
-    unsigned short* kwt  = (unsigned short*)(ws + 1363972);
+    float* lpart = ws + 327680;
+    float* hpart = ws + 344064;
+    float* gpart = ws + 393216;
+    float* wsum  = ws + 458752;
+    int*   mode  = (int*)(ws + 458760);
+    int*   cnt   = (int*)(ws + 458761);
+    int*   gen   = (int*)(ws + 458762);
+    unsigned short* uw1t = (unsigned short*)(ws + 458764);
+    unsigned short* uw2t = (unsigned short*)(ws + 753676);
+    unsigned short* g2t  = (unsigned short*)(ws + 851980);
+    unsigned short* g1t  = (unsigned short*)(ws + 876556);
+    unsigned short* kwt  = (unsigned short*)(ws + 901132);
     float* out   = (float*)d_out;
 
     k_prep<<<489, 256, 0, stream>>>(uw1, uw2, gw2, gw1, kw,
                                     (const unsigned char*)adj,
-                                    lc, cw, cb, lpw,
-                                    uw1t, uw2t, g2t, g1t, kwt, mode, lpart);
-    k_npp<<<BB * NN_ / 16, 256, 0, stream>>>(nf, pnw, pnb, g1t, gb1, h, preg);
-    for (int i = 0; i < NG; ++i) {
-        const float* gw1i = gw1 + (size_t)i * 259 * EH;
-        float* out2sel = (i == NG - 1) ? (out + 1040) : (float*)nullptr;
-        const unsigned short* g1tn = (i < NG - 1) ? (g1t + (size_t)(i + 1) * 16384)
-                                                  : (const unsigned short*)nullptr;
-        const float* gb1n = (i < NG - 1) ? (gb1 + (i + 1) * EH) : (const float*)nullptr;
-        k_edge<<<BB * NN_, 256, 0, stream>>>(h, preg, ef, adj, mode, gw1i,
-                                             g2t + (size_t)i * 16384,
-                                             gb2 + i * DD, amean, amax);
-        k_updp<<<BB * NN_ / 4, 256, 0, stream>>>(h, amean, amax,
-                                                 uw1t + (size_t)i * 196608, ub1 + i * DD,
-                                                 uw2t + (size_t)i * 65536, ub2 + i * DD,
-                                                 lng + i * DD, lnb + i * DD, h, out2sel,
-                                                 g1tn, gb1n, preg);
-    }
-    k_gembed<<<BB, 256, 0, stream>>>(nf, h, ge);
-    k_hmm<<<96, 256, 0, stream>>>(ge, gd, qw, sw1, vw1, lpb, lpart, hpart);
-    k_scr<<<BB * NN_ / 16, 256, 0, stream>>>(h, kwt, kb, hpart, qb, sb1, vb1,
-                                             sw2, sb2, vw2, vb2, out);
+                                    lc, cw, cb, lpw, nf,
+                                    uw1t, uw2t, g2t, g1t, kwt, mode, lpart, wsum, cnt);
+    k_mega<<<NBLK, 256, 0, stream>>>(nf, ef, adj, gd, pnw, pnb,
+                                     gw1, gb1, gb2, ub1, ub2, lng, lnb,
+                                     qw, sw1, vw1, qb, sb1, vb1,
+                                     sw2, sb2, vw2, vb2, kb, lpb,
+                                     h, preg, lpart, hpart, gpart, wsum,
+                                     mode, cnt, gen, uw1t, uw2t, g2t, g1t, kwt, out);
 }
```

Result: slower. 597.7 us (+225.0%).
